# Optimization experiments

Measured on AMD Instinct MI355X. Metric: run time of the kernel, lower is better.

The kernel has to match this reference:

```python
import jax, jax.numpy as jnp
import numpy as np

B, L, E, H, W = 2, 4096, 512, 8, 128
D = E // H

def _clin(x, Wr, Wi, br, bi):
    # ComplexLinear on real input: out = x@(Wr + i*Wi)^T + (br + i*bi)
    return x @ Wr.T + br, x @ Wi.T + bi

def setup_inputs() -> dict:
    key = jax.random.key(0)
    ks = jax.random.split(key, 20)
    s = 0.02
    d = {
        'query': jax.random.normal(ks[0], (B, L, E), jnp.float32),
        'key':   jax.random.normal(ks[1], (B, L, E), jnp.float32),
        'value': jax.random.normal(ks[2], (B, L, E), jnp.float32),
    }
    names = ['q', 'k', 'v', 'o']
    i = 3
    for n in names:
        d[n + 'Wr'] = jax.random.normal(ks[i], (E, E), jnp.float32) * s; i += 1
        d[n + 'Wi'] = jax.random.normal(ks[i], (E, E), jnp.float32) * s; i += 1
        d[n + 'br'] = jnp.zeros((E,), jnp.float32)
        d[n + 'bi'] = jnp.zeros((E,), jnp.float32)
    return d

def reference(query, key, value,
              qWr, qWi, qbr, qbi,
              kWr, kWi, kbr, kbi,
              vWr, vWi, vbr, vbi,
              oWr, oWi, obr, obi):
    # complex projections (real input -> complex output, kept as (re, im) float pairs)
    qr, qi = _clin(query, qWr, qWi, qbr, qbi)
    kr, ki = _clin(key,   kWr, kWi, kbr, kbi)
    vr, _vi = _clin(value, vWr, vWi, vbr, vbi)  # imag part of V is discarded by the real cast

    def heads(x):
        return x.reshape(B, L, H, D).transpose(0, 2, 1, 3)  # [B,H,L,D]
    qr, qi, kr, ki, vr = map(heads, (qr, qi, kr, ki, vr))

    # Re(q @ k^H) = qr@kr^T + qi@ki^T  (only the real part is ever used)
    scale = 1.0 / np.sqrt(D)
    scores = (jnp.einsum('bhld,bhmd->bhlm', qr, kr)
              + jnp.einsum('bhld,bhmd->bhlm', qi, ki)) * scale

    # Faithful to source: only lower_mask is applied (window_mask is built but never added).
    idx = jnp.arange(L)
    lower_mask = jnp.where(idx[:, None] - idx[None, :] >= W + 1,
                           -jnp.inf, 0.0).astype(scores.dtype)
    probs = jax.nn.softmax(scores + lower_mask, axis=-1)

    # out = probs @ v; cast to query.dtype keeps only Re = probs @ vr
    o = jnp.einsum('bhlm,bhmd->bhld', probs, vr)
    o = o.transpose(0, 2, 1, 3).reshape(B, L, E)

    out_r = o @ oWr.T + obr
    out_i = o @ oWi.T + obi
    return out_r, out_i
```

## Files before the change

kernel.cpp:

```cpp
#include <hip/hip_runtime.h>


typedef unsigned short u16;
typedef unsigned int u32;
typedef __attribute__((ext_vector_type(8))) short bf16x8;
typedef __attribute__((ext_vector_type(4))) float f32x4;
typedef __attribute__((ext_vector_type(16))) float f32x16;
typedef __attribute__((ext_vector_type(4))) u32 u32x4;

#define L_ 4096
#define E_ 512
#define M_ 8192

__device__ __forceinline__ u16 f2bf(float f) {
  union { float f; u32 u; } v; v.f = f;
  return (u16)((v.u + 0x7FFFu + ((v.u >> 16) & 1u)) >> 16);
}

__device__ __forceinline__ float fexp2(float x) {
  float r;
  asm("v_exp_f32 %0, %1" : "=v"(r) : "v"(x));
  return r;
}

__device__ __forceinline__ void gll16(const void* g, void* l) {
  __builtin_amdgcn_global_load_lds(
      (const __attribute__((address_space(1))) u32*)g,
      (__attribute__((address_space(3))) u32*)l, 16, 0, 0);
}

__global__ void cvt_x_kernel(const float* __restrict__ q, const float* __restrict__ k,
                             const float* __restrict__ v,
                             u16* __restrict__ xq, u16* __restrict__ xk, u16* __restrict__ xv) {
  const int total = 3 * (M_ * E_ / 4);
  int stride = gridDim.x * blockDim.x;
  for (int u = blockIdx.x * blockDim.x + threadIdx.x; u < total; u += stride) {
    int mat = u >> 20, e = u & ((1 << 20) - 1);
    const float4 f = ((const float4*)(mat == 0 ? q : mat == 1 ? k : v))[e];
    ushort4 o = make_ushort4(f2bf(f.x), f2bf(f.y), f2bf(f.z), f2bf(f.w));
    *(ushort4*)((mat == 0 ? xq : mat == 1 ? xk : xv) + (size_t)e * 4) = o;
  }
}

struct CPtrs { const float* w[7]; const float* b[7]; };

__global__ void cvt_wb_kernel(CPtrs p, u16* __restrict__ wcat, float* __restrict__ bcat) {
  const int total = 7 * (E_ * E_ / 4);
  int stride = gridDim.x * blockDim.x;
  int t0 = blockIdx.x * blockDim.x + threadIdx.x;
  for (int u = t0; u < total; u += stride) {
    int wi = u >> 16, e = u & 65535;
    const float4 f = ((const float4*)p.w[wi])[e];
    ushort4 o = make_ushort4(f2bf(f.x), f2bf(f.y), f2bf(f.z), f2bf(f.w));
    *(ushort4*)(wcat + (size_t)wi * 262144 + (size_t)e * 4) = o;
  }
  for (int j = t0; j < 3584; j += stride) bcat[j] = p.b[j >> 9][j & 511];
}

__device__ __forceinline__ void gemm128_main(const u16* __restrict__ A, const u16* __restrict__ Bw,
                                             int m0, int n0w, char* sm, f32x4 acc[4][4]) {
  int tid = threadIdx.x;
  int lane = tid & 63, w = tid >> 6;
  int wm = w >> 1, wn = w & 1;
#pragma unroll
  for (int a = 0; a < 4; a++)
#pragma unroll
    for (int b = 0; b < 4; b++)
#pragma unroll
      for (int j = 0; j < 4; j++) acc[a][b][j] = 0.f;

  auto stage = [&](int buf, int ks) {
    char* dst = sm + buf * 16384;
#pragma unroll
    for (int n = 0; n < 2; n++) {
      int u = n * 256 + tid;
      int row = u >> 2, c = u & 3;
      int so = (c ^ (row & 3)) * 16;
      int ldso = (n * 256 + w * 64) * 16;
      gll16((const char*)(A + (size_t)(m0 + row) * 512 + ks * 32) + so, dst + ldso);
      gll16((const char*)(Bw + (size_t)(n0w + row) * 512 + ks * 32) + so, dst + 8192 + ldso);
    }
  };

  stage(0, 0);
  __syncthreads();
  int cur = 0;
  for (int ks = 0; ks < 16; ks++) {
    if (ks < 15) stage(cur ^ 1, ks + 1);
    const char* as = sm + cur * 16384;
    const char* bs = as + 8192;
    bf16x8 af[4], bfr[4];
#pragma unroll
    for (int i = 0; i < 4; i++) {
      int ra = wm * 64 + i * 16 + (lane & 15);
      af[i] = *(const bf16x8*)(as + ra * 64 + (((lane >> 4) * 16) ^ ((ra & 3) << 4)));
      int rb = wn * 64 + i * 16 + (lane & 15);
      bfr[i] = *(const bf16x8*)(bs + rb * 64 + (((lane >> 4) * 16) ^ ((rb & 3) << 4)));
    }
    __builtin_amdgcn_s_setprio(1);
#pragma unroll
    for (int mt = 0; mt < 4; mt++)
#pragma unroll
      for (int nt = 0; nt < 4; nt++)
        acc[mt][nt] = __builtin_amdgcn_mfma_f32_16x16x32_bf16(af[mt], bfr[nt], acc[mt][nt], 0, 0, 0);
    __builtin_amdgcn_s_setprio(0);
    __syncthreads();
    cur ^= 1;
  }
}

__global__ __launch_bounds__(256) void proj_kernel(
    const u16* __restrict__ xq, const u16* __restrict__ xk, const u16* __restrict__ xv,
    const u16* __restrict__ wcat, const float* __restrict__ bcat,
    u16* __restrict__ qrb, u16* __restrict__ qib,
    u16* __restrict__ krb, u16* __restrict__ kib, u16* __restrict__ vtb) {
  __shared__ alignas(16) char sm[32768];
  int bx = blockIdx.x, by = blockIdx.y;
  const u16* A = bx < 8 ? xq : (bx < 16 ? xk : xv);
  int m0 = by * 128, n0w = bx * 128;
  f32x4 acc[4][4];
  gemm128_main(A, wcat, m0, n0w, sm, acc);

  int lane = threadIdx.x & 63, w = threadIdx.x >> 6;
  int wm = w >> 1, wn = w & 1;
  int lL = lane & 15, lH = lane >> 4;
#pragma unroll
  for (int mt = 0; mt < 4; mt++) {
#pragma unroll
    for (int nt = 0; nt < 4; nt++) {
      int n = n0w + wn * 64 + nt * 16 + lL;
      float bias = bcat[n];
      int e = n & 511;
#pragma unroll
      for (int j = 0; j < 4; j++) {
        int m = m0 + wm * 64 + mt * 16 + lH * 4 + j;
        float val = acc[mt][nt][j] + bias;
        int bb = m >> 12, ll = m & 4095;
        if (bx < 16) {
          if (bx < 8) val *= 0.18033688011112042f;
          u16* dst = (bx < 8) ? ((n & 512) ? qib : qrb) : ((n & 512) ? kib : krb);
          dst[((size_t)((bb * 8 + (e >> 6)) * 4096 + ll) << 6) + (e & 63)] = f2bf(val);
        } else {
          vtb[((size_t)((bb * 8 + (e >> 6)) * 64 + (e & 63)) << 12) + ll] = f2bf(val);
        }
      }
    }
  }
}

__global__ __launch_bounds__(256) void oproj_kernel(
    const u16* __restrict__ obf, const u16* __restrict__ wcat, const float* __restrict__ bcat,
    float* __restrict__ out) {
  __shared__ alignas(16) char sm[32768];
  int bx = blockIdx.x, by = blockIdx.y;
  int m0 = by * 128, n0w = 2560 + bx * 128;
  f32x4 acc[4][4];
  gemm128_main(obf, wcat, m0, n0w, sm, acc);

  int lane = threadIdx.x & 63, w = threadIdx.x >> 6;
  int wm = w >> 1, wn = w & 1;
  int lL = lane & 15, lH = lane >> 4;
#pragma unroll
  for (int mt = 0; mt < 4; mt++) {
#pragma unroll
    for (int nt = 0; nt < 4; nt++) {
      int n = n0w + wn * 64 + nt * 16 + lL;
      float bias = bcat[n];
      int nn = n - 2560;
      float* dst = out + ((nn & 512) ? 4194304 : 0) + (nn & 511);
#pragma unroll
      for (int j = 0; j < 4; j++) {
        int m = m0 + wm * 64 + mt * 16 + lH * 4 + j;
        dst[(size_t)m * 512] = acc[mt][nt][j] + bias;
      }
    }
  }
}

__global__ __launch_bounds__(256, 3) void attn_kernel(
    const u16* __restrict__ qrb, const u16* __restrict__ qib,
    const u16* __restrict__ krb, const u16* __restrict__ kib,
    const u16* __restrict__ vtb, u16* __restrict__ obf) {
  __shared__ alignas(16) char sm[49152];
  int bid = blockIdx.x;
  int bh = bid & 15;
  int qt = bid >> 4;
  int bb = bh >> 3, hh = bh & 7;
  int i0 = qt << 6;
  int tid = threadIdx.x;
  int lane = tid & 63, w = tid >> 6;
  int grp = w >> 1, wq = w & 1;
  int lo = lane & 31, hi = lane >> 5;
  int i0w = i0 + wq * 32;
  int irow = i0w + lo;

  int jstart = (i0 >= 128) ? (i0 - 128) : 0;
  int ntiles = (4096 - jstart) >> 5;
  int nper = ntiles >> 1;

  bf16x8 fqr[4], fqi[4];
  {
    const u16* qp = qrb + ((size_t)(bh * 4096 + irow) << 6) + hi * 8;
    const u16* qip = qib + ((size_t)(bh * 4096 + irow) << 6) + hi * 8;
#pragma unroll
    for (int c = 0; c < 4; c++) {
      fqr[c] = *(const bf16x8*)(qp + c * 16);
      fqi[c] = *(const bf16x8*)(qip + c * 16);
    }
  }

  const char* gp[6];
  int adv[6], ldso[6];
  {
    const char* krbB = (const char*)krb + ((size_t)(bh * 4096 + jstart) << 7);
    const char* kibB = (const char*)kib + ((size_t)(bh * 4096 + jstart) << 7);
    const char* vtbB = (const char*)vtb + ((size_t)(bh * 64) << 13) + ((size_t)jstart << 1);
#pragma unroll
    for (int s = 0; s < 6; s++) {
      int cc = 6 * w + s;
      ldso[s] = cc << 10;
      if (cc < 16) {
        int tI = cc >> 3;
        int kind = (cc >> 2) & 1;
        int r = (cc & 3) * 8 + (lane >> 3);
        int so = ((lane & 7) ^ (r & 7)) << 4;
        gp[s] = (kind ? kibB : krbB) + (size_t)(tI * 32 + r) * 128 + so;
        adv[s] = 8192;
      } else {
        int dr = (cc - 16) * 8 + (lane >> 3);
        int so = ((lane & 7) ^ (dr & 7)) << 4;
        gp[s] = vtbB + (size_t)dr * 8192 + so;
        adv[s] = 128;
      }
    }
  }
  auto stagep = [&](char* dst) {
#pragma unroll
    for (int s = 0; s < 6; s++) {
      gll16(gp[s], dst + ldso[s]);
      gp[s] += adv[s];
    }
  };

  int swz = (lo & 7) << 4;
  int offK[4], offVT[2];
#pragma unroll
  for (int c = 0; c < 4; c++) offK[c] = lo * 128 + ((c * 32 + hi * 16) ^ swz);
#pragma unroll
  for (int kc = 0; kc < 2; kc++)
    offVT[kc] = 16384 + lo * 128 + ((grp * 64 + kc * 32 + hi * 16) ^ swz);

  auto cvtpk = [](float a, float b) -> u32 {
    u32 r;
    asm("v_cvt_pk_bf16_f32 %0, %1, %2" : "=v"(r) : "v"(a), "v"(b));
    return r;
  };

  f32x16 oa0, oa1;
#pragma unroll
  for (int r = 0; r < 16; r++) { oa0[r] = 0.f; oa1[r] = 0.f; }
  float l_run = 0.f;
  const int iband = irow - 129;

  stagep(sm);
  __syncthreads();
  int j0g = jstart + grp * 32;

  for (int p = 0; p < nper; p++) {
    char* half = sm + (p & 1) * 24576;
    if (p + 1 < nper) stagep(sm + ((p + 1) & 1) * 24576);
    const char* Kr = half + grp * 8192;
    const char* Ki = Kr + 4096;

    f32x16 s0;
#pragma unroll
    for (int r = 0; r < 16; r++) s0[r] = 0.f;
#pragma unroll
    for (int c = 0; c < 4; c++) {
      bf16x8 ar = *(const bf16x8*)(Kr + offK[c]);
      bf16x8 ai = *(const bf16x8*)(Ki + offK[c]);
      __builtin_amdgcn_s_setprio(1);
      s0 = __builtin_amdgcn_mfma_f32_32x32x16_bf16(ar, fqr[c], s0, 0, 0, 0);
      s0 = __builtin_amdgcn_mfma_f32_32x32x16_bf16(ai, fqi[c], s0, 0, 0, 0);
      __builtin_amdgcn_s_setprio(0);
    }
    if (j0g <= i0w - 98) {
#pragma unroll
      for (int r = 0; r < 16; r++) {
        int kk = j0g + (r & 3) + ((r >> 2) << 3) + (hi << 2);
        if (kk <= iband) s0[r] = -3e38f;
      }
    }
    float ps0 = 0.f, ps1 = 0.f, ps2 = 0.f, ps3 = 0.f;
#pragma unroll
    for (int r = 0; r < 16; r += 4) {
      s0[r] = fexp2(s0[r]);         ps0 += s0[r];
      s0[r + 1] = fexp2(s0[r + 1]); ps1 += s0[r + 1];
      s0[r + 2] = fexp2(s0[r + 2]); ps2 += s0[r + 2];
      s0[r + 3] = fexp2(s0[r + 3]); ps3 += s0[r + 3];
    }
    float psum = (ps0 + ps1) + (ps2 + ps3);
    psum += __shfl_xor(psum, 32);
    l_run += psum;

    bf16x8 pf0, pf1;
    {
      const float* pp = (const float*)&s0;
      u32 x0 = cvtpk(pp[0], pp[1]), y0 = cvtpk(pp[4], pp[5]);
      u32 x1 = cvtpk(pp[2], pp[3]), y1 = cvtpk(pp[6], pp[7]);
      u32 x2 = cvtpk(pp[8], pp[9]), y2 = cvtpk(pp[12], pp[13]);
      u32 x3 = cvtpk(pp[10], pp[11]), y3 = cvtpk(pp[14], pp[15]);
      asm("v_permlane32_swap_b32 %0, %1" : "+v"(x0), "+v"(y0));
      asm("v_permlane32_swap_b32 %0, %1" : "+v"(x1), "+v"(y1));
      asm("v_permlane32_swap_b32 %0, %1" : "+v"(x2), "+v"(y2));
      asm("v_permlane32_swap_b32 %0, %1" : "+v"(x3), "+v"(y3));
      u32x4 a; a[0] = x0; a[1] = x1; a[2] = y0; a[3] = y1;
      u32x4 b; b[0] = x2; b[1] = x3; b[2] = y2; b[3] = y3;
      pf0 = __builtin_bit_cast(bf16x8, a);
      pf1 = __builtin_bit_cast(bf16x8, b);
    }
    {
      bf16x8 av00 = *(const bf16x8*)(half + offVT[0]);
      bf16x8 av01 = *(const bf16x8*)(half + offVT[0] + 4096);
      bf16x8 av10 = *(const bf16x8*)(half + offVT[1]);
      bf16x8 av11 = *(const bf16x8*)(half + offVT[1] + 4096);
      __builtin_amdgcn_s_setprio(1);
      oa0 = __builtin_amdgcn_mfma_f32_32x32x16_bf16(av00, pf0, oa0, 0, 0, 0);
      oa1 = __builtin_amdgcn_mfma_f32_32x32x16_bf16(av01, pf0, oa1, 0, 0, 0);
      oa0 = __builtin_amdgcn_mfma_f32_32x32x16_bf16(av10, pf1, oa0, 0, 0, 0);
      oa1 = __builtin_amdgcn_mfma_f32_32x32x16_bf16(av11, pf1, oa1, 0, 0, 0);
      __builtin_amdgcn_s_setprio(0);
    }
    j0g += 64;
    __syncthreads();
  }

  int swo = (lo & 7) << 4;
  char* ob = sm + wq * 8192;
  if (grp == 1) {
#pragma unroll
    for (int g2 = 0; g2 < 4; g2++) {
      f32x4 v0; f32x4 v1;
#pragma unroll
      for (int e = 0; e < 4; e++) { v0[e] = oa0[4 * g2 + e]; v1[e] = oa1[4 * g2 + e]; }
      *(f32x4*)(ob + lo * 256 + ((g2 * 32 + hi * 16) ^ swo)) = v0;
      *(f32x4*)(ob + lo * 256 + ((128 + g2 * 32 + hi * 16) ^ swo)) = v1;
    }
    if (!hi) *(float*)(sm + 16384 + wq * 128 + lo * 4) = l_run;
  }
  __syncthreads();
  if (grp == 0) {
    float l2 = *(const float*)(sm + 16384 + wq * 128 + lo * 4);
    float rl = 1.0f / (l_run + l2);
    u16* orow = obf + ((size_t)(bb * 4096 + irow) << 9) + hh * 64;
#pragma unroll
    for (int g2 = 0; g2 < 4; g2++) {
      f32x4 v0 = *(const f32x4*)(ob + lo * 256 + ((g2 * 32 + hi * 16) ^ swo));
      f32x4 v1 = *(const f32x4*)(ob + lo * 256 + ((128 + g2 * 32 + hi * 16) ^ swo));
      ushort4 o0 = make_ushort4(f2bf((oa0[4 * g2] + v0[0]) * rl),
                                f2bf((oa0[4 * g2 + 1] + v0[1]) * rl),
                                f2bf((oa0[4 * g2 + 2] + v0[2]) * rl),
                                f2bf((oa0[4 * g2 + 3] + v0[3]) * rl));
      *(ushort4*)(orow + g2 * 8 + hi * 4) = o0;
      ushort4 o1 = make_ushort4(f2bf((oa1[4 * g2] + v1[0]) * rl),
                                f2bf((oa1[4 * g2 + 1] + v1[1]) * rl),
                                f2bf((oa1[4 * g2 + 2] + v1[2]) * rl),
                                f2bf((oa1[4 * g2 + 3] + v1[3]) * rl));
      *(ushort4*)(orow + 32 + g2 * 8 + hi * 4) = o1;
    }
  }
}

extern "C" void kernel_launch(void* const* d_in, const int* in_sizes, int n_in,
                              void* d_out, int out_size, void* d_ws, size_t ws_size,
                              hipStream_t stream) {
  (void)in_sizes; (void)n_in; (void)out_size; (void)ws_size;
  const float* q = (const float*)d_in[0];
  const float* k = (const float*)d_in[1];
  const float* v = (const float*)d_in[2];
  char* ws = (char*)d_ws;
  u16* wcat = (u16*)(ws + 0x000000);
  float* bcat = (float*)(ws + 0x400000);
  u16* xq  = (u16*)(ws + 0x500000);
  u16* xk  = (u16*)(ws + 0xD00000);
  u16* xv  = (u16*)(ws + 0x1500000);
  u16* qrb = (u16*)(ws + 0x1D00000);
  u16* qib = (u16*)(ws + 0x2500000);
  u16* krb = (u16*)(ws + 0x2D00000);
  u16* kib = (u16*)(ws + 0x3500000);
  u16* vtb = (u16*)(ws + 0x3D00000);
  u16* obf = xq;
  float* out = (float*)d_out;

  cvt_x_kernel<<<2048, 256, 0, stream>>>(q, k, v, xq, xk, xv);

  CPtrs cp;
  cp.w[0] = (const float*)d_in[3];  cp.w[1] = (const float*)d_in[4];
  cp.w[2] = (const float*)d_in[7];  cp.w[3] = (const float*)d_in[8];
  cp.w[4] = (const float*)d_in[11]; cp.w[5] = (const float*)d_in[15]; cp.w[6] = (const float*)d_in[16];
  cp.b[0] = (const float*)d_in[5];  cp.b[1] = (const float*)d_in[6];
  cp.b[2] = (const float*)d_in[9];  cp.b[3] = (const float*)d_in[10];
  cp.b[4] = (const float*)d_in[13]; cp.b[5] = (const float*)d_in[17]; cp.b[6] = (const float*)d_in[18];
  cvt_wb_kernel<<<448, 256, 0, stream>>>(cp, wcat, bcat);

  proj_kernel<<<dim3(20, 64), 256, 0, stream>>>(xq, xk, xv, wcat, bcat, qrb, qib, krb, kib, vtb);
  attn_kernel<<<1024, 256, 0, stream>>>(qrb, qib, krb, kib, vtb, obf);
  oproj_kernel<<<dim3(8, 64), 256, 0, stream>>>(obf, wcat, bcat, out);
}
```

Before: 166.5 us.

## Single-buffer K and double-buffer V in attention, merge conversion kernels

The attention kernel's shared-memory footprint shrinks from 48KB to 32KB. K is now single-buffered and restaged after a mid-iteration barrier, while V stays double-buffered, and the launch-bounds occupancy hint is raised from 3 to 5 blocks. The input and weight bf16 conversion kernels are merged into one launch that splits work by block index. The aim is more resident blocks per CU and one less kernel launch, at the cost of an extra barrier per iteration and less prefetch lead time for K.

```diff
diff --git a/kernel.cpp b/kernel.cpp
--- a/kernel.cpp
+++ b/kernel.cpp
@@ -29,32 +29,34 @@
       (__attribute__((address_space(3))) u32*)l, 16, 0, 0);
 }
 
-__global__ void cvt_x_kernel(const float* __restrict__ q, const float* __restrict__ k,
-                             const float* __restrict__ v,
-                             u16* __restrict__ xq, u16* __restrict__ xk, u16* __restrict__ xv) {
-  const int total = 3 * (M_ * E_ / 4);
-  int stride = gridDim.x * blockDim.x;
-  for (int u = blockIdx.x * blockDim.x + threadIdx.x; u < total; u += stride) {
-    int mat = u >> 20, e = u & ((1 << 20) - 1);
-    const float4 f = ((const float4*)(mat == 0 ? q : mat == 1 ? k : v))[e];
-    ushort4 o = make_ushort4(f2bf(f.x), f2bf(f.y), f2bf(f.z), f2bf(f.w));
-    *(ushort4*)((mat == 0 ? xq : mat == 1 ? xk : xv) + (size_t)e * 4) = o;
-  }
-}
-
 struct CPtrs { const float* w[7]; const float* b[7]; };
 
-__global__ void cvt_wb_kernel(CPtrs p, u16* __restrict__ wcat, float* __restrict__ bcat) {
-  const int total = 7 * (E_ * E_ / 4);
-  int stride = gridDim.x * blockDim.x;
-  int t0 = blockIdx.x * blockDim.x + threadIdx.x;
-  for (int u = t0; u < total; u += stride) {
-    int wi = u >> 16, e = u & 65535;
-    const float4 f = ((const float4*)p.w[wi])[e];
-    ushort4 o = make_ushort4(f2bf(f.x), f2bf(f.y), f2bf(f.z), f2bf(f.w));
-    *(ushort4*)(wcat + (size_t)wi * 262144 + (size_t)e * 4) = o;
-  }
-  for (int j = t0; j < 3584; j += stride) bcat[j] = p.b[j >> 9][j & 511];
+__global__ void cvt_all_kernel(const float* __restrict__ q, const float* __restrict__ k,
+                               const float* __restrict__ v, CPtrs p,
+                               u16* __restrict__ xq, u16* __restrict__ xk, u16* __restrict__ xv,
+                               u16* __restrict__ wcat, float* __restrict__ bcat) {
+  int bid = blockIdx.x;
+  if (bid < 2048) {
+    const int total = 3 * (M_ * E_ / 4);
+    const int stride = 2048 * 256;
+    for (int u = bid * 256 + threadIdx.x; u < total; u += stride) {
+      int mat = u >> 20, e = u & ((1 << 20) - 1);
+      const float4 f = ((const float4*)(mat == 0 ? q : mat == 1 ? k : v))[e];
+      ushort4 o = make_ushort4(f2bf(f.x), f2bf(f.y), f2bf(f.z), f2bf(f.w));
+      *(ushort4*)((mat == 0 ? xq : mat == 1 ? xk : xv) + (size_t)e * 4) = o;
+    }
+  } else {
+    const int total = 7 * (E_ * E_ / 4);
+    const int stride = 448 * 256;
+    int t0 = (bid - 2048) * 256 + threadIdx.x;
+    for (int u = t0; u < total; u += stride) {
+      int wi = u >> 16, e = u & 65535;
+      const float4 f = ((const float4*)p.w[wi])[e];
+      ushort4 o = make_ushort4(f2bf(f.x), f2bf(f.y), f2bf(f.z), f2bf(f.w));
+      *(ushort4*)(wcat + (size_t)wi * 262144 + (size_t)e * 4) = o;
+    }
+    for (int j = t0; j < 3584; j += stride) bcat[j] = p.b[j >> 9][j & 511];
+  }
 }
 
 __device__ __forceinline__ void gemm128_main(const u16* __restrict__ A, const u16* __restrict__ Bw,
@@ -177,11 +179,11 @@
   }
 }
 
-__global__ __launch_bounds__(256, 3) void attn_kernel(
+__global__ __launch_bounds__(256, 5) void attn_kernel(
     const u16* __restrict__ qrb, const u16* __restrict__ qib,
     const u16* __restrict__ krb, const u16* __restrict__ kib,
     const u16* __restrict__ vtb, u16* __restrict__ obf) {
-  __shared__ alignas(16) char sm[49152];
+  __shared__ alignas(16) char sm[32768];
   int bid = blockIdx.x;
   int bh = bid & 15;
   int qt = bid >> 4;
@@ -209,43 +211,46 @@
     }
   }
 
-  const char* gp[6];
-  int adv[6], ldso[6];
+  const char* gpk[4];
+  int ldk[4];
+  const char* gpv[2];
+  int ldv[2];
   {
     const char* krbB = (const char*)krb + ((size_t)(bh * 4096 + jstart) << 7);
     const char* kibB = (const char*)kib + ((size_t)(bh * 4096 + jstart) << 7);
     const char* vtbB = (const char*)vtb + ((size_t)(bh * 64) << 13) + ((size_t)jstart << 1);
 #pragma unroll
-    for (int s = 0; s < 6; s++) {
-      int cc = 6 * w + s;
-      ldso[s] = cc << 10;
-      if (cc < 16) {
-        int tI = cc >> 3;
-        int kind = (cc >> 2) & 1;
-        int r = (cc & 3) * 8 + (lane >> 3);
-        int so = ((lane & 7) ^ (r & 7)) << 4;
-        gp[s] = (kind ? kibB : krbB) + (size_t)(tI * 32 + r) * 128 + so;
-        adv[s] = 8192;
-      } else {
-        int dr = (cc - 16) * 8 + (lane >> 3);
-        int so = ((lane & 7) ^ (dr & 7)) << 4;
-        gp[s] = vtbB + (size_t)dr * 8192 + so;
-        adv[s] = 128;
-      }
-    }
-  }
-  auto stagep = [&](char* dst) {
-#pragma unroll
-    for (int s = 0; s < 6; s++) {
-      gll16(gp[s], dst + ldso[s]);
-      gp[s] += adv[s];
-    }
+    for (int s = 0; s < 4; s++) {
+      int cc = 4 * w + s;
+      int tI = cc >> 3;
+      int kind = (cc >> 2) & 1;
+      int r = (cc & 3) * 8 + (lane >> 3);
+      int so = ((lane & 7) ^ (r & 7)) << 4;
+      gpk[s] = (kind ? kibB : krbB) + (size_t)(tI * 32 + r) * 128 + so;
+      ldk[s] = cc << 10;
+    }
+#pragma unroll
+    for (int s = 0; s < 2; s++) {
+      int cc = 2 * w + s;
+      int dr = cc * 8 + (lane >> 3);
+      int so = ((lane & 7) ^ (dr & 7)) << 4;
+      gpv[s] = vtbB + (size_t)dr * 8192 + so;
+      ldv[s] = 16384 + (cc << 10);
+    }
+  }
+  auto stageK = [&]() {
+#pragma unroll
+    for (int s = 0; s < 4; s++) { gll16(gpk[s], sm + ldk[s]); gpk[s] += 8192; }
+  };
+  auto stageV = [&](int buf) {
+#pragma unroll
+    for (int s = 0; s < 2; s++) { gll16(gpv[s], sm + buf * 8192 + ldv[s]); gpv[s] += 128; }
   };
 
   int swz = (lo & 7) << 4;
   int offK[4], offVT[2];
 #pragma unroll
-  for (int c = 0; c < 4; c++) offK[c] = lo * 128 + ((c * 32 + hi * 16) ^ swz);
+  for (int c = 0; c < 4; c++) offK[c] = grp * 8192 + lo * 128 + ((c * 32 + hi * 16) ^ swz);
 #pragma unroll
   for (int kc = 0; kc < 2; kc++)
     offVT[kc] = 16384 + lo * 128 + ((grp * 64 + kc * 32 + hi * 16) ^ swz);
@@ -262,28 +267,29 @@
   float l_run = 0.f;
   const int iband = irow - 129;
 
-  stagep(sm);
+  stageK();
+  stageV(0);
   __syncthreads();
   int j0g = jstart + grp * 32;
 
   for (int p = 0; p < nper; p++) {
-    char* half = sm + (p & 1) * 24576;
-    if (p + 1 < nper) stagep(sm + ((p + 1) & 1) * 24576);
-    const char* Kr = half + grp * 8192;
-    const char* Ki = Kr + 4096;
+    if (p + 1 < nper) stageV((p + 1) & 1);
 
     f32x16 s0;
 #pragma unroll
     for (int r = 0; r < 16; r++) s0[r] = 0.f;
 #pragma unroll
     for (int c = 0; c < 4; c++) {
-      bf16x8 ar = *(const bf16x8*)(Kr + offK[c]);
-      bf16x8 ai = *(const bf16x8*)(Ki + offK[c]);
+      bf16x8 ar = *(const bf16x8*)(sm + offK[c]);
+      bf16x8 ai = *(const bf16x8*)(sm + 4096 + offK[c]);
       __builtin_amdgcn_s_setprio(1);
       s0 = __builtin_amdgcn_mfma_f32_32x32x16_bf16(ar, fqr[c], s0, 0, 0, 0);
       s0 = __builtin_amdgcn_mfma_f32_32x32x16_bf16(ai, fqi[c], s0, 0, 0, 0);
       __builtin_amdgcn_s_setprio(0);
     }
+    __syncthreads();
+    if (p + 1 < nper) stageK();
+
     if (j0g <= i0w - 98) {
 #pragma unroll
       for (int r = 0; r < 16; r++) {
@@ -320,10 +326,11 @@
       pf1 = __builtin_bit_cast(bf16x8, b);
     }
     {
-      bf16x8 av00 = *(const bf16x8*)(half + offVT[0]);
-      bf16x8 av01 = *(const bf16x8*)(half + offVT[0] + 4096);
-      bf16x8 av10 = *(const bf16x8*)(half + offVT[1]);
-      bf16x8 av11 = *(const bf16x8*)(half + offVT[1] + 4096);
+      const char* vb = sm + (p & 1) * 8192;
+      bf16x8 av00 = *(const bf16x8*)(vb + offVT[0]);
+      bf16x8 av01 = *(const bf16x8*)(vb + offVT[0] + 4096);
+      bf16x8 av10 = *(const bf16x8*)(vb + offVT[1]);
+      bf16x8 av11 = *(const bf16x8*)(vb + offVT[1] + 4096);
       __builtin_amdgcn_s_setprio(1);
       oa0 = __builtin_amdgcn_mfma_f32_32x32x16_bf16(av00, pf0, oa0, 0, 0, 0);
       oa1 = __builtin_amdgcn_mfma_f32_32x32x16_bf16(av01, pf0, oa1, 0, 0, 0);
@@ -392,8 +399,6 @@
   u16* obf = xq;
   float* out = (float*)d_out;
 
-  cvt_x_kernel<<<2048, 256, 0, stream>>>(q, k, v, xq, xk, xv);
-
   CPtrs cp;
   cp.w[0] = (const float*)d_in[3];  cp.w[1] = (const float*)d_in[4];
   cp.w[2] = (const float*)d_in[7];  cp.w[3] = (const float*)d_in[8];
@@ -401,8 +406,8 @@
   cp.b[0] = (const float*)d_in[5];  cp.b[1] = (const float*)d_in[6];
   cp.b[2] = (const float*)d_in[9];  cp.b[3] = (const float*)d_in[10];
   cp.b[4] = (const float*)d_in[13]; cp.b[5] = (const float*)d_in[17]; cp.b[6] = (const float*)d_in[18];
-  cvt_wb_kernel<<<448, 256, 0, stream>>>(cp, wcat, bcat);
-
+
+  cvt_all_kernel<<<2496, 256, 0, stream>>>(q, k, v, cp, xq, xk, xv, wcat, bcat);
   proj_kernel<<<dim3(20, 64), 256, 0, stream>>>(xq, xk, xv, wcat, bcat, qrb, qib, krb, kib, vtb);
   attn_kernel<<<1024, 256, 0, stream>>>(qrb, qib, krb, kib, vtb, obf);
   oproj_kernel<<<dim3(8, 64), 256, 0, stream>>>(obf, wcat, bcat, out);
```

New measurement: 304.0 us. +82.6%, slower.
